# Kernel optimization log

Hardware: AMD Instinct MI355X
Metric: run time of the kernel (lower is better)

The kernel has to match this reference:

```python
import jax, jax.numpy as jnp
import numpy as np

N_POINTS = 262144
L_LEVELS = 16
FEATS_PER_LEVEL = 2
BASE_RES = 8
FINEST_RES = 512
TABLE_SIZE = 2 ** 12  # log2_hashmap_size = 12
HIDDEN = 256
IN_FEATURES = 3
MLP_IN = L_LEVELS * FEATS_PER_LEVEL + IN_FEATURES - 2  # 33


def _level_params():
    b = np.exp((np.log(FINEST_RES) - np.log(BASE_RES)) / (L_LEVELS - 1))
    res = np.floor(BASE_RES * b ** np.arange(L_LEVELS)).astype(np.int64)
    hsize = np.minimum(res ** 2, TABLE_SIZE)  # per-level hashmap size
    return jnp.asarray(res, jnp.float32), jnp.asarray(hsize, jnp.uint32)


RES, HSIZE = _level_params()
PRIMES = jnp.array([1, 2654435761], dtype=jnp.uint32)  # instant-NGP spatial hash primes (2D)
CORNERS = jnp.array([[0, 0], [0, 1], [1, 0], [1, 1]], dtype=jnp.int32)  # [4,2]


def hash_encode(coords, tables):
    # coords: [N,2] in [0,1]; tables: [L, TABLE_SIZE, F]
    x = coords[None, :, :] * RES[:, None, None]            # [L,N,2] scaled per level
    xi = jnp.floor(x)
    xf = x - xi                                            # fractional part (grad flows to coords)
    inds = xi.astype(jnp.int32)[:, :, None, :] + CORNERS   # [L,N,4,2] corner integer coords
    # bilinear weights: offset 0 -> (1-xf), offset 1 -> xf
    w = jnp.prod(jnp.where(CORNERS == 0, 1.0 - xf[:, :, None, :], xf[:, :, None, :]), axis=-1)  # [L,N,4]
    u = inds.astype(jnp.uint32) * PRIMES                   # [L,N,4,2]
    h = (u[..., 0] ^ u[..., 1]) % HSIZE[:, None, None]     # [L,N,4] hashed table index
    feats = jax.vmap(lambda t, i: t[i])(tables, h)         # [L,N,4,F] gather per level
    out = jnp.einsum('lncf,lnc->lnf', feats, w)            # [L,N,F] bilinear interp
    return jnp.moveaxis(out, 0, 1).reshape(coords.shape[0], -1)  # [N, L*F], level-major per point


def reference(x, tables, W0, b0, W1, b1, W2, b2, W3, b3, W4, b4):
    h = hash_encode(x[:, :2], tables)                      # [N, 32]
    h = jnp.concatenate([h, x[:, 2:]], axis=-1)            # [N, 33]
    h = jax.nn.relu(h @ W0 + b0)
    h = jax.nn.relu(h @ W1 + b1)
    h = jax.nn.relu(h @ W2 + b2)
    h = jax.nn.relu(h @ W3 + b3)
    return h @ W4 + b4                                     # [N, 1]


def setup_inputs() -> dict:
    key = jax.random.key(0)
    ks = jax.random.split(key, 12)

    def lin(kw, fan_in, fan_out):
        s = 1.0 / np.sqrt(fan_in)
        return jax.random.normal(kw, (fan_in, fan_out), jnp.float32) * s

    return {
        'x': jax.random.uniform(ks[0], (N_POINTS, IN_FEATURES), jnp.float32),
        'tables': jax.random.normal(ks[1], (L_LEVELS, TABLE_SIZE, FEATS_PER_LEVEL), jnp.float32) * 1e-2,
        'W0': lin(ks[2], MLP_IN, HIDDEN), 'b0': jnp.zeros((HIDDEN,), jnp.float32),
        'W1': lin(ks[3], HIDDEN, HIDDEN), 'b1': jnp.zeros((HIDDEN,), jnp.float32),
        'W2': lin(ks[4], HIDDEN, HIDDEN), 'b2': jnp.zeros((HIDDEN,), jnp.float32),
        'W3': lin(ks[5], HIDDEN, HIDDEN), 'b3': jnp.zeros((HIDDEN,), jnp.float32),
        'W4': lin(ks[6], HIDDEN, 1),      'b4': jnp.zeros((1,), jnp.float32),
    }
```

## Files before the change

kernel.cpp:

```cpp
#include <hip/hip_runtime.h>
#include <math.h>


typedef __bf16 bf16x8 __attribute__((ext_vector_type(8)));
typedef float  f32x4  __attribute__((ext_vector_type(4)));
typedef unsigned int u32x4 __attribute__((ext_vector_type(4)));
typedef unsigned int u32x2 __attribute__((ext_vector_type(2)));

struct LevelParams {
  float res[16];
  unsigned hsize[16];
  unsigned M[8];
  unsigned c16[8];
  int      sh[8];
};

static constexpr int MTILE = 64;
static constexpr int LDA   = 264;
static constexpr int ACT_ELEMS = MTILE * LDA;
static constexpr int UNITS_L0 = 32;
static constexpr int UB_L0 = 0, UB_L1 = 32, UB_L2 = 160, UB_L3 = 288;
static constexpr int UNITS_TOTAL = 416;

__device__ __forceinline__ unsigned short f32_to_bf16_rne(float f) {
  unsigned u = __float_as_uint(f);
  unsigned r = (u + 0x7fffu + ((u >> 16) & 1u)) >> 16;
  return (unsigned short)r;
}
__device__ __forceinline__ float bf16_bits_to_f32(unsigned u16bits) {
  return __uint_as_float(u16bits << 16);
}

__device__ __forceinline__ unsigned pack_hi(unsigned u0, unsigned u1) {
  return (u0 >> 16) | (u1 & 0xffff0000u);
}

__global__ void prep_pack(const float* __restrict__ W0, const float* __restrict__ W1,
                          const float* __restrict__ W2, const float* __restrict__ W3,
                          unsigned short* __restrict__ pack) {
  int b = blockIdx.x;
  int lane = threadIdx.x;
  const float* W; int K; int r;
  if (b < UNITS_L0) { W = W0; K = 33; r = b; }
  else {
    int b2 = b - UNITS_L0; int ly = b2 >> 7; r = b2 & 127;
    W = (ly == 0) ? W1 : (ly == 1) ? W2 : W3; K = 256;
  }
  int s = r >> 4, ct = r & 15;
  int col   = (ct << 4) + (lane & 15);
  int kbase = (s << 5) + ((lane >> 4) << 3);
  unsigned short* dst = pack + (size_t)b * 1024;
#pragma unroll
  for (int e = 0; e < 8; ++e) {
    int k = kbase + e;
    float v = (k < K) ? W[k * 256 + col] : 0.0f;
    unsigned u = __float_as_uint(v);
    unsigned short h = (unsigned short)(u >> 16);
    float hf = bf16_bits_to_f32(u >> 16);
    unsigned short lo = f32_to_bf16_rne(v - hf);
    dst[lane * 8 + e]       = h;
    dst[512 + lane * 8 + e] = lo;
  }
}

template<int S>
__device__ __forceinline__ void run_layer(unsigned short* __restrict__ ahi,
                                          unsigned short* __restrict__ alo,
                                          const unsigned short* __restrict__ pack,
                                          int unitbase,
                                          const float* __restrict__ bias,
                                          int wc, int lm, int lg, int lane) {
  f32x4 acc[4][2];
#pragma unroll
  for (int i = 0; i < 4; ++i)
#pragma unroll
    for (int j = 0; j < 2; ++j) acc[i][j] = (f32x4)0.0f;

#pragma unroll
  for (int s = 0; s < S; ++s) {
    bf16x8 w_h[2], w_l[2];
#pragma unroll
    for (int ct = 0; ct < 2; ++ct) {
      const unsigned short* bp =
          pack + (size_t)(unitbase + (s << 4) + (wc << 1) + ct) * 1024 + (lane << 3);
      w_h[ct] = __builtin_bit_cast(bf16x8, *(const u32x4*)(bp));
      w_l[ct] = __builtin_bit_cast(bf16x8, *(const u32x4*)(bp + 512));
    }
#pragma unroll
    for (int pt = 0; pt < 4; ++pt) {
      int off = ((pt << 4) + lm) * LDA + (s << 5) + (lg << 3);
      bf16x8 a_h = __builtin_bit_cast(bf16x8, *(const u32x4*)(ahi + off));
      bf16x8 a_l = __builtin_bit_cast(bf16x8, *(const u32x4*)(alo + off));
      acc[pt][0] = __builtin_amdgcn_mfma_f32_16x16x32_bf16(w_h[0], a_h, acc[pt][0], 0, 0, 0);
      acc[pt][1] = __builtin_amdgcn_mfma_f32_16x16x32_bf16(w_h[1], a_h, acc[pt][1], 0, 0, 0);
      acc[pt][0] = __builtin_amdgcn_mfma_f32_16x16x32_bf16(w_l[0], a_h, acc[pt][0], 0, 0, 0);
      acc[pt][1] = __builtin_amdgcn_mfma_f32_16x16x32_bf16(w_l[1], a_h, acc[pt][1], 0, 0, 0);
      acc[pt][0] = __builtin_amdgcn_mfma_f32_16x16x32_bf16(w_h[0], a_l, acc[pt][0], 0, 0, 0);
      acc[pt][1] = __builtin_amdgcn_mfma_f32_16x16x32_bf16(w_h[1], a_l, acc[pt][1], 0, 0, 0);
    }
  }
  __syncthreads();
#pragma unroll
  for (int pt = 0; pt < 4; ++pt)
#pragma unroll
    for (int ct = 0; ct < 2; ++ct) {
      int colbase = (((wc << 1) + ct) << 4) + (lg << 2);
      float4 bv = *(const float4*)(bias + colbase);
      int base = ((pt << 4) + lm) * LDA + colbase;
      float v0 = fmaxf(acc[pt][ct][0] + bv.x, 0.0f);
      float v1 = fmaxf(acc[pt][ct][1] + bv.y, 0.0f);
      float v2 = fmaxf(acc[pt][ct][2] + bv.z, 0.0f);
      float v3 = fmaxf(acc[pt][ct][3] + bv.w, 0.0f);
      unsigned u0 = __float_as_uint(v0), u1 = __float_as_uint(v1);
      unsigned u2 = __float_as_uint(v2), u3 = __float_as_uint(v3);
      u32x2 hw = { pack_hi(u0, u1), pack_hi(u2, u3) };
      float l0 = v0 - __uint_as_float(u0 & 0xffff0000u);
      float l1 = v1 - __uint_as_float(u1 & 0xffff0000u);
      float l2 = v2 - __uint_as_float(u2 & 0xffff0000u);
      float l3 = v3 - __uint_as_float(u3 & 0xffff0000u);
      u32x2 lw = { pack_hi(__float_as_uint(l0), __float_as_uint(l1)),
                   pack_hi(__float_as_uint(l2), __float_as_uint(l3)) };
      *(u32x2*)(ahi + base) = hw;
      *(u32x2*)(alo + base) = lw;
    }
  __syncthreads();
}

__global__ __launch_bounds__(512, 4) void inr_main(
    const float* __restrict__ x, const float* __restrict__ tables,
    const float* __restrict__ b0, const float* __restrict__ b1,
    const float* __restrict__ b2, const float* __restrict__ b3,
    const float* __restrict__ W4, const float* __restrict__ b4,
    const unsigned short* __restrict__ pack, float* __restrict__ out,
    LevelParams P) {
  extern __shared__ char smem[];
  unsigned short* ahi = (unsigned short*)smem;
  unsigned short* alo = ahi + ACT_ELEMS;

  const int tid = threadIdx.x;

  {
    int pl = tid >> 3, q = tid & 7;
    size_t p = (size_t)blockIdx.x * MTILE + pl;
    float x0 = x[3 * p + 0], x1 = x[3 * p + 1], x2 = x[3 * p + 2];
    float f_lo0, f_lo1, f_hi0, f_hi1;

    {
      float rf = P.res[q];
      unsigned d = P.hsize[q], c = P.c16[q], M = P.M[q];
      int sh = P.sh[q];
      float xs0 = x0 * rf, xs1 = x1 * rf;
      float fl0 = floorf(xs0), fl1 = floorf(xs1);
      float f0 = xs0 - fl0, f1 = xs1 - fl1;
      int i0 = (int)fl0, i1 = (int)fl1;
      unsigned ua0 = (unsigned)i0, ua1 = (unsigned)(i0 + 1);
      unsigned vb0 = (unsigned)i1 * 2654435761u;
      unsigned vb1 = (unsigned)(i1 + 1) * 2654435761u;
      const float* tl = tables + ((size_t)q << 13);
      float g0 = 1.0f - f0, g1 = 1.0f - f1;
      unsigned e0 = ua0 ^ vb0, e1 = ua0 ^ vb1, e2 = ua1 ^ vb0, e3 = ua1 ^ vb1;
      unsigned n0 = (e0 >> 16) * c + (e0 & 0xffffu);
      unsigned n1 = (e1 >> 16) * c + (e1 & 0xffffu);
      unsigned n2 = (e2 >> 16) * c + (e2 & 0xffffu);
      unsigned n3 = (e3 >> 16) * c + (e3 & 0xffffu);
      unsigned h0 = n0 - (__umulhi(n0, M) >> sh) * d;
      unsigned h1 = n1 - (__umulhi(n1, M) >> sh) * d;
      unsigned h2 = n2 - (__umulhi(n2, M) >> sh) * d;
      unsigned h3 = n3 - (__umulhi(n3, M) >> sh) * d;
      float a0 = 0.0f, a1 = 0.0f;
      { float w = g0 * g1; a0 += w * tl[2*h0]; a1 += w * tl[2*h0+1]; }
      { float w = g0 * f1; a0 += w * tl[2*h1]; a1 += w * tl[2*h1+1]; }
      { float w = f0 * g1; a0 += w * tl[2*h2]; a1 += w * tl[2*h2+1]; }
      { float w = f0 * f1; a0 += w * tl[2*h3]; a1 += w * tl[2*h3+1]; }
      f_lo0 = a0; f_lo1 = a1;
    }
    {
      int l = q + 8;
      float rf = P.res[l];
      float xs0 = x0 * rf, xs1 = x1 * rf;
      float fl0 = floorf(xs0), fl1 = floorf(xs1);
      float f0 = xs0 - fl0, f1 = xs1 - fl1;
      int i0 = (int)fl0, i1 = (int)fl1;
      unsigned ua0 = (unsigned)i0, ua1 = (unsigned)(i0 + 1);
      unsigned vb0 = (unsigned)i1 * 2654435761u;
      unsigned vb1 = (unsigned)(i1 + 1) * 2654435761u;
      const float* tl = tables + ((size_t)l << 13);
      float g0 = 1.0f - f0, g1 = 1.0f - f1;
      unsigned h0 = (ua0 ^ vb0) & 4095u, h1 = (ua0 ^ vb1) & 4095u;
      unsigned h2 = (ua1 ^ vb0) & 4095u, h3 = (ua1 ^ vb1) & 4095u;
      float a0 = 0.0f, a1 = 0.0f;
      { float w = g0 * g1; a0 += w * tl[2*h0]; a1 += w * tl[2*h0+1]; }
      { float w = g0 * f1; a0 += w * tl[2*h1]; a1 += w * tl[2*h1+1]; }
      { float w = f0 * g1; a0 += w * tl[2*h2]; a1 += w * tl[2*h2+1]; }
      { float w = f0 * f1; a0 += w * tl[2*h3]; a1 += w * tl[2*h3+1]; }
      f_hi0 = a0; f_hi1 = a1;
    }
    {
      int rowb = pl * LDA;
      unsigned u0 = __float_as_uint(f_lo0), u1 = __float_as_uint(f_lo1);
      unsigned u2 = __float_as_uint(f_hi0), u3 = __float_as_uint(f_hi1);
      float l0 = f_lo0 - __uint_as_float(u0 & 0xffff0000u);
      float l1 = f_lo1 - __uint_as_float(u1 & 0xffff0000u);
      float l2 = f_hi0 - __uint_as_float(u2 & 0xffff0000u);
      float l3 = f_hi1 - __uint_as_float(u3 & 0xffff0000u);
      *(unsigned*)(ahi + rowb + 2*q)      = pack_hi(u0, u1);
      *(unsigned*)(ahi + rowb + 16 + 2*q) = pack_hi(u2, u3);
      *(unsigned*)(alo + rowb + 2*q)      = pack_hi(__float_as_uint(l0), __float_as_uint(l1));
      *(unsigned*)(alo + rowb + 16 + 2*q) = pack_hi(__float_as_uint(l2), __float_as_uint(l3));
    }
    {
      int base = pl * LDA + 32 + (q << 2);
      if (q == 0) {
        unsigned u0 = __float_as_uint(x2);
        float l0 = x2 - __uint_as_float(u0 & 0xffff0000u);
        u32x2 hw = { u0 >> 16, 0u };
        u32x2 lw = { __float_as_uint(l0) >> 16, 0u };
        *(u32x2*)(ahi + base) = hw;
        *(u32x2*)(alo + base) = lw;
      } else {
        u32x2 z = { 0u, 0u };
        *(u32x2*)(ahi + base) = z;
        *(u32x2*)(alo + base) = z;
      }
    }
  }
  __syncthreads();

  const int lane = tid & 63;
  const int wc = tid >> 6;
  const int lm = lane & 15, lg = lane >> 4;

  run_layer<2>(ahi, alo, pack, UB_L0, b0, wc, lm, lg, lane);
  run_layer<8>(ahi, alo, pack, UB_L1, b1, wc, lm, lg, lane);
  run_layer<8>(ahi, alo, pack, UB_L2, b2, wc, lm, lg, lane);
  run_layer<8>(ahi, alo, pack, UB_L3, b3, wc, lm, lg, lane);

  {
    int pl = tid >> 3, q = tid & 7;
    const unsigned short* hrow = ahi + pl * LDA + (q << 5);
    const unsigned short* lrow = alo + pl * LDA + (q << 5);
    const float* w4p = W4 + (q << 5);
    float sum = 0.0f;
#pragma unroll
    for (int c = 0; c < 4; ++c) {
      u32x4 th = *(const u32x4*)(hrow + (c << 3));
      u32x4 tl = *(const u32x4*)(lrow + (c << 3));
      float4 wA = *(const float4*)(w4p + (c << 3));
      float4 wB = *(const float4*)(w4p + (c << 3) + 4);
#pragma unroll
      for (int u = 0; u < 4; ++u) {
        unsigned hu = th[u], lu = tl[u];
        float v0 = __uint_as_float(hu << 16) + __uint_as_float(lu << 16);
        float v1 = __uint_as_float(hu & 0xffff0000u) + __uint_as_float(lu & 0xffff0000u);
        const float* wp = (u < 2) ? &wA.x : &wB.x;
        int base = (u & 1) << 1;
        sum = fmaf(v0, wp[base], sum);
        sum = fmaf(v1, wp[base + 1], sum);
      }
    }
    sum += __shfl_xor(sum, 1);
    sum += __shfl_xor(sum, 2);
    sum += __shfl_xor(sum, 4);
    if (q == 0) out[(size_t)blockIdx.x * MTILE + pl] = sum + b4[0];
  }
}

extern "C" void kernel_launch(void* const* d_in, const int* in_sizes, int n_in,
                              void* d_out, int out_size, void* d_ws, size_t ws_size,
                              hipStream_t stream) {
  const float* x      = (const float*)d_in[0];
  const float* tables = (const float*)d_in[1];
  const float* W0 = (const float*)d_in[2];  const float* b0 = (const float*)d_in[3];
  const float* W1 = (const float*)d_in[4];  const float* b1 = (const float*)d_in[5];
  const float* W2 = (const float*)d_in[6];  const float* b2 = (const float*)d_in[7];
  const float* W3 = (const float*)d_in[8];  const float* b3 = (const float*)d_in[9];
  const float* W4 = (const float*)d_in[10]; const float* b4 = (const float*)d_in[11];
  unsigned short* pack = (unsigned short*)d_ws;
  float* out = (float*)d_out;

  LevelParams P;
  double bgrow = exp((log(512.0) - log(8.0)) / 15.0);
  for (int l = 0; l < 16; ++l) {
    double r = floor(8.0 * pow(bgrow, (double)l));
    P.res[l] = (float)r;
    double hsd = r * r;
    if (hsd > 4096.0) hsd = 4096.0;
    P.hsize[l] = (unsigned)hsd;
  }
  for (int l = 0; l < 8; ++l) {
    unsigned d = P.hsize[l];
    P.c16[l] = 65536u % d;
    unsigned long long nmax = 65535ULL * d;
    int s = 0;
    while (nmax * d >= (1ULL << (32 + s))) s++;
    P.sh[l] = s;
    P.M[l] = (unsigned)((1ULL << (32 + s)) / d + 1);
  }

  prep_pack<<<UNITS_TOTAL, 64, 0, stream>>>(W0, W1, W2, W3, pack);

  size_t smem_bytes = (size_t)ACT_ELEMS * 2 * 2;
  hipFuncSetAttribute(reinterpret_cast<const void*>(inr_main),
                      hipFuncAttributeMaxDynamicSharedMemorySize, (int)smem_bytes);

  int nblocks = out_size / MTILE;
  inr_main<<<nblocks, 512, smem_bytes, stream>>>(x, tables, b0, b1, b2, b3, W4, b4,
                                                 pack, out, P);
}
```

Baseline: 287.7 us.

## Switch MLP layers to 32x32x16 MFMA with register-prefetched weight fragments

Replaces the 16x16x32 bf16 MFMA tiling (each wave covering 32 columns in four 16-row tiles) with 32x32x16 MFMA, where each wave owns 32 output columns across two 32-row tiles. The weight pack layout is rebuilt to match: 16-deep K steps, 32 columns per unit, and fewer padded units for layer 0. Weight fragments for the next K step are loaded into registers before the current step's MFMAs run, to hide global-load latency. The larger MFMA reads fewer LDS activation fragments per FLOP, but the 16-wide accumulators raise register pressure at 4 blocks per CU.

Result: slower. 308.9 us (+7.4%).

```diff
diff --git a/kernel.cpp b/kernel.cpp
--- a/kernel.cpp
+++ b/kernel.cpp
@@ -3,7 +3,7 @@
 
 
 typedef __bf16 bf16x8 __attribute__((ext_vector_type(8)));
-typedef float  f32x4  __attribute__((ext_vector_type(4)));
+typedef float  f32x16 __attribute__((ext_vector_type(16)));
 typedef unsigned int u32x4 __attribute__((ext_vector_type(4)));
 typedef unsigned int u32x2 __attribute__((ext_vector_type(2)));
 
@@ -18,9 +18,8 @@
 static constexpr int MTILE = 64;
 static constexpr int LDA   = 264;
 static constexpr int ACT_ELEMS = MTILE * LDA;
-static constexpr int UNITS_L0 = 32;
-static constexpr int UB_L0 = 0, UB_L1 = 32, UB_L2 = 160, UB_L3 = 288;
-static constexpr int UNITS_TOTAL = 416;
+static constexpr int UB_L0 = 0, UB_L1 = 24, UB_L2 = 152, UB_L3 = 280;
+static constexpr int UNITS_TOTAL = 408;
 
 __device__ __forceinline__ unsigned short f32_to_bf16_rne(float f) {
   unsigned u = __float_as_uint(f);
@@ -30,7 +29,6 @@
 __device__ __forceinline__ float bf16_bits_to_f32(unsigned u16bits) {
   return __uint_as_float(u16bits << 16);
 }
-
 __device__ __forceinline__ unsigned pack_hi(unsigned u0, unsigned u1) {
   return (u0 >> 16) | (u1 & 0xffff0000u);
 }
@@ -39,27 +37,26 @@
                           const float* __restrict__ W2, const float* __restrict__ W3,
                           unsigned short* __restrict__ pack) {
   int b = blockIdx.x;
-  int lane = threadIdx.x;
-  const float* W; int K; int r;
-  if (b < UNITS_L0) { W = W0; K = 33; r = b; }
+  int l = threadIdx.x;
+  const float* W; int K, s, cq;
+  if (b < UB_L1) { W = W0; K = 33; s = b >> 3; cq = b & 7; }
   else {
-    int b2 = b - UNITS_L0; int ly = b2 >> 7; r = b2 & 127;
-    W = (ly == 0) ? W1 : (ly == 1) ? W2 : W3; K = 256;
-  }
-  int s = r >> 4, ct = r & 15;
-  int col   = (ct << 4) + (lane & 15);
-  int kbase = (s << 5) + ((lane >> 4) << 3);
-  unsigned short* dst = pack + (size_t)b * 1024;
+    int b2 = b - UB_L1; int ly = b2 >> 7; int r = b2 & 127;
+    W = (ly == 0) ? W1 : (ly == 1) ? W2 : W3; K = 256; s = r >> 3; cq = r & 7;
+  }
+  int col = (cq << 5) + (l & 31);
+  int kb  = (s << 4) + ((l >> 5) << 3);
+  unsigned short* dst = pack + (size_t)b * 1024 + l * 8;
 #pragma unroll
   for (int e = 0; e < 8; ++e) {
-    int k = kbase + e;
+    int k = kb + e;
     float v = (k < K) ? W[k * 256 + col] : 0.0f;
     unsigned u = __float_as_uint(v);
     unsigned short h = (unsigned short)(u >> 16);
     float hf = bf16_bits_to_f32(u >> 16);
     unsigned short lo = f32_to_bf16_rne(v - hf);
-    dst[lane * 8 + e]       = h;
-    dst[512 + lane * 8 + e] = lo;
+    dst[e]       = h;
+    dst[512 + e] = lo;
   }
 }
 
@@ -67,50 +64,55 @@
 __device__ __forceinline__ void run_layer(unsigned short* __restrict__ ahi,
                                           unsigned short* __restrict__ alo,
                                           const unsigned short* __restrict__ pack,
-                                          int unitbase,
+                                          int ubase,
                                           const float* __restrict__ bias,
-                                          int wc, int lm, int lg, int lane) {
-  f32x4 acc[4][2];
-#pragma unroll
-  for (int i = 0; i < 4; ++i)
-#pragma unroll
-    for (int j = 0; j < 2; ++j) acc[i][j] = (f32x4)0.0f;
-
+                                          int cq, int l) {
+  f32x16 acc0 = (f32x16)0.0f, acc1 = (f32x16)0.0f;
+  const int i31 = l & 31, p = l >> 5;
+
+  const unsigned short* a0h = ahi + i31 * LDA + (p << 3);
+  const unsigned short* a1h = ahi + (32 + i31) * LDA + (p << 3);
+  const unsigned short* a0l = alo + i31 * LDA + (p << 3);
+  const unsigned short* a1l = alo + (32 + i31) * LDA + (p << 3);
+  const unsigned short* wb  = pack + (size_t)(ubase + cq) * 1024 + l * 8;
+
+  u32x4 wh = *(const u32x4*)(wb);
+  u32x4 wl = *(const u32x4*)(wb + 512);
 #pragma unroll
   for (int s = 0; s < S; ++s) {
-    bf16x8 w_h[2], w_l[2];
-#pragma unroll
-    for (int ct = 0; ct < 2; ++ct) {
-      const unsigned short* bp =
-          pack + (size_t)(unitbase + (s << 4) + (wc << 1) + ct) * 1024 + (lane << 3);
-      w_h[ct] = __builtin_bit_cast(bf16x8, *(const u32x4*)(bp));
-      w_l[ct] = __builtin_bit_cast(bf16x8, *(const u32x4*)(bp + 512));
-    }
-#pragma unroll
-    for (int pt = 0; pt < 4; ++pt) {
-      int off = ((pt << 4) + lm) * LDA + (s << 5) + (lg << 3);
-      bf16x8 a_h = __builtin_bit_cast(bf16x8, *(const u32x4*)(ahi + off));
-      bf16x8 a_l = __builtin_bit_cast(bf16x8, *(const u32x4*)(alo + off));
-      acc[pt][0] = __builtin_amdgcn_mfma_f32_16x16x32_bf16(w_h[0], a_h, acc[pt][0], 0, 0, 0);
-      acc[pt][1] = __builtin_amdgcn_mfma_f32_16x16x32_bf16(w_h[1], a_h, acc[pt][1], 0, 0, 0);
-      acc[pt][0] = __builtin_amdgcn_mfma_f32_16x16x32_bf16(w_l[0], a_h, acc[pt][0], 0, 0, 0);
-      acc[pt][1] = __builtin_amdgcn_mfma_f32_16x16x32_bf16(w_l[1], a_h, acc[pt][1], 0, 0, 0);
-      acc[pt][0] = __builtin_amdgcn_mfma_f32_16x16x32_bf16(w_h[0], a_l, acc[pt][0], 0, 0, 0);
-      acc[pt][1] = __builtin_amdgcn_mfma_f32_16x16x32_bf16(w_h[1], a_l, acc[pt][1], 0, 0, 0);
-    }
+    u32x4 whn = wh, wln = wl;
+    if (s + 1 < S) {
+      whn = *(const u32x4*)(wb + (size_t)(s + 1) * 8192);
+      wln = *(const u32x4*)(wb + (size_t)(s + 1) * 8192 + 512);
+    }
+    bf16x8 ah0 = __builtin_bit_cast(bf16x8, *(const u32x4*)(a0h + (s << 4)));
+    bf16x8 al0 = __builtin_bit_cast(bf16x8, *(const u32x4*)(a0l + (s << 4)));
+    bf16x8 ah1 = __builtin_bit_cast(bf16x8, *(const u32x4*)(a1h + (s << 4)));
+    bf16x8 al1 = __builtin_bit_cast(bf16x8, *(const u32x4*)(a1l + (s << 4)));
+    bf16x8 W_h = __builtin_bit_cast(bf16x8, wh);
+    bf16x8 W_l = __builtin_bit_cast(bf16x8, wl);
+    acc0 = __builtin_amdgcn_mfma_f32_32x32x16_bf16(W_h, ah0, acc0, 0, 0, 0);
+    acc1 = __builtin_amdgcn_mfma_f32_32x32x16_bf16(W_h, ah1, acc1, 0, 0, 0);
+    acc0 = __builtin_amdgcn_mfma_f32_32x32x16_bf16(W_l, ah0, acc0, 0, 0, 0);
+    acc1 = __builtin_amdgcn_mfma_f32_32x32x16_bf16(W_l, ah1, acc1, 0, 0, 0);
+    acc0 = __builtin_amdgcn_mfma_f32_32x32x16_bf16(W_h, al0, acc0, 0, 0, 0);
+    acc1 = __builtin_amdgcn_mfma_f32_32x32x16_bf16(W_h, al1, acc1, 0, 0, 0);
+    wh = whn; wl = wln;
   }
   __syncthreads();
-#pragma unroll
-  for (int pt = 0; pt < 4; ++pt)
-#pragma unroll
-    for (int ct = 0; ct < 2; ++ct) {
-      int colbase = (((wc << 1) + ct) << 4) + (lg << 2);
-      float4 bv = *(const float4*)(bias + colbase);
-      int base = ((pt << 4) + lm) * LDA + colbase;
-      float v0 = fmaxf(acc[pt][ct][0] + bv.x, 0.0f);
-      float v1 = fmaxf(acc[pt][ct][1] + bv.y, 0.0f);
-      float v2 = fmaxf(acc[pt][ct][2] + bv.z, 0.0f);
-      float v3 = fmaxf(acc[pt][ct][3] + bv.w, 0.0f);
+
+#pragma unroll
+  for (int pt = 0; pt < 2; ++pt) {
+    int arow = (pt << 5) + i31;
+    f32x16 A = pt ? acc1 : acc0;
+#pragma unroll
+    for (int g = 0; g < 4; ++g) {
+      int chb = (cq << 5) + (g << 3) + (p << 2);
+      float4 bv = *(const float4*)(bias + chb);
+      float v0 = fmaxf(A[4 * g + 0] + bv.x, 0.0f);
+      float v1 = fmaxf(A[4 * g + 1] + bv.y, 0.0f);
+      float v2 = fmaxf(A[4 * g + 2] + bv.z, 0.0f);
+      float v3 = fmaxf(A[4 * g + 3] + bv.w, 0.0f);
       unsigned u0 = __float_as_uint(v0), u1 = __float_as_uint(v1);
       unsigned u2 = __float_as_uint(v2), u3 = __float_as_uint(v3);
       u32x2 hw = { pack_hi(u0, u1), pack_hi(u2, u3) };
@@ -120,9 +122,11 @@
       float l3 = v3 - __uint_as_float(u3 & 0xffff0000u);
       u32x2 lw = { pack_hi(__float_as_uint(l0), __float_as_uint(l1)),
                    pack_hi(__float_as_uint(l2), __float_as_uint(l3)) };
+      int base = arow * LDA + chb;
       *(u32x2*)(ahi + base) = hw;
       *(u32x2*)(alo + base) = lw;
     }
+  }
   __syncthreads();
 }
 
@@ -141,8 +145,8 @@
 
   {
     int pl = tid >> 3, q = tid & 7;
-    size_t p = (size_t)blockIdx.x * MTILE + pl;
-    float x0 = x[3 * p + 0], x1 = x[3 * p + 1], x2 = x[3 * p + 2];
+    size_t pidx = (size_t)blockIdx.x * MTILE + pl;
+    float x0 = x[3 * pidx + 0], x1 = x[3 * pidx + 1], x2 = x[3 * pidx + 2];
     float f_lo0, f_lo1, f_hi0, f_hi1;
 
     {
@@ -175,8 +179,8 @@
       f_lo0 = a0; f_lo1 = a1;
     }
     {
-      int l = q + 8;
-      float rf = P.res[l];
+      int lv = q + 8;
+      float rf = P.res[lv];
       float xs0 = x0 * rf, xs1 = x1 * rf;
       float fl0 = floorf(xs0), fl1 = floorf(xs1);
       float f0 = xs0 - fl0, f1 = xs1 - fl1;
@@ -184,7 +188,7 @@
       unsigned ua0 = (unsigned)i0, ua1 = (unsigned)(i0 + 1);
       unsigned vb0 = (unsigned)i1 * 2654435761u;
       unsigned vb1 = (unsigned)(i1 + 1) * 2654435761u;
-      const float* tl = tables + ((size_t)l << 13);
+      const float* tl = tables + ((size_t)lv << 13);
       float g0 = 1.0f - f0, g1 = 1.0f - f1;
       unsigned h0 = (ua0 ^ vb0) & 4095u, h1 = (ua0 ^ vb1) & 4095u;
       unsigned h2 = (ua1 ^ vb0) & 4095u, h3 = (ua1 ^ vb1) & 4095u;
@@ -209,31 +213,27 @@
       *(unsigned*)(alo + rowb + 16 + 2*q) = pack_hi(__float_as_uint(l2), __float_as_uint(l3));
     }
     {
-      int base = pl * LDA + 32 + (q << 2);
+      int base = pl * LDA + 32 + 2*q;
       if (q == 0) {
         unsigned u0 = __float_as_uint(x2);
         float l0 = x2 - __uint_as_float(u0 & 0xffff0000u);
-        u32x2 hw = { u0 >> 16, 0u };
-        u32x2 lw = { __float_as_uint(l0) >> 16, 0u };
-        *(u32x2*)(ahi + base) = hw;
-        *(u32x2*)(alo + base) = lw;
+        *(unsigned*)(ahi + base) = u0 >> 16;
+        *(unsigned*)(alo + base) = __float_as_uint(l0) >> 16;
       } else {
-        u32x2 z = { 0u, 0u };
-        *(u32x2*)(ahi + base) = z;
-        *(u32x2*)(alo + base) = z;
+        *(unsigned*)(ahi + base) = 0u;
+        *(unsigned*)(alo + base) = 0u;
       }
     }
   }
   __syncthreads();
 
-  const int lane = tid & 63;
-  const int wc = tid >> 6;
-  const int lm = lane & 15, lg = lane >> 4;
-
-  run_layer<2>(ahi, alo, pack, UB_L0, b0, wc, lm, lg, lane);
-  run_layer<8>(ahi, alo, pack, UB_L1, b1, wc, lm, lg, lane);
-  run_layer<8>(ahi, alo, pack, UB_L2, b2, wc, lm, lg, lane);
-  run_layer<8>(ahi, alo, pack, UB_L3, b3, wc, lm, lg, lane);
+  const int l  = tid & 63;
+  const int cq = tid >> 6;
+
+  run_layer<3>(ahi, alo, pack, UB_L0, b0, cq, l);
+  run_layer<16>(ahi, alo, pack, UB_L1, b1, cq, l);
+  run_layer<16>(ahi, alo, pack, UB_L2, b2, cq, l);
+  run_layer<16>(ahi, alo, pack, UB_L3, b3, cq, l);
 
   {
     int pl = tid >> 3, q = tid & 7;
@@ -280,21 +280,21 @@
 
   LevelParams P;
   double bgrow = exp((log(512.0) - log(8.0)) / 15.0);
-  for (int l = 0; l < 16; ++l) {
-    double r = floor(8.0 * pow(bgrow, (double)l));
-    P.res[l] = (float)r;
+  for (int lvl = 0; lvl < 16; ++lvl) {
+    double r = floor(8.0 * pow(bgrow, (double)lvl));
+    P.res[lvl] = (float)r;
     double hsd = r * r;
     if (hsd > 4096.0) hsd = 4096.0;
-    P.hsize[l] = (unsigned)hsd;
-  }
-  for (int l = 0; l < 8; ++l) {
-    unsigned d = P.hsize[l];
-    P.c16[l] = 65536u % d;
+    P.hsize[lvl] = (unsigned)hsd;
+  }
+  for (int lvl = 0; lvl < 8; ++lvl) {
+    unsigned d = P.hsize[lvl];
+    P.c16[lvl] = 65536u % d;
     unsigned long long nmax = 65535ULL * d;
     int s = 0;
     while (nmax * d >= (1ULL << (32 + s))) s++;
-    P.sh[l] = s;
-    P.M[l] = (unsigned)((1ULL << (32 + s)) / d + 1);
+    P.sh[lvl] = s;
+    P.M[lvl] = (unsigned)((1ULL << (32 + s)) / d + 1);
   }
 
   prep_pack<<<UNITS_TOTAL, 64, 0, stream>>>(W0, W1, W2, W3, pack);
```
